# Kernel optimization log

Hardware: AMD Instinct MI355X
Metric: run time of the kernel (lower is better)

The kernel has to match this reference:

```python
import jax, jax.numpy as jnp
import numpy as np

HIDDEN = 1024
IN = 256
OUT = 256
DT_OVER_TAU = 0.05  # dt=0.05, tau=1


def setup_inputs() -> dict:
    key = jax.random.key(0)
    k0, k1, k2, k3 = jax.random.split(key, 4)
    g = 0.9
    x = jax.random.normal(k0, (512, 64, IN), dtype=jnp.float32)  # (tsq, batch, n_input)
    Win = jax.random.normal(k1, (IN, HIDDEN), dtype=jnp.float32) * (1.0 / HIDDEN)
    Wr = jax.random.normal(k2, (HIDDEN, HIDDEN), dtype=jnp.float32) * (g * g / HIDDEN)
    bias = jnp.zeros((1, HIDDEN), dtype=jnp.float32)
    Wout = jax.random.normal(k3, (HIDDEN, OUT), dtype=jnp.float32) * (1.0 / HIDDEN)
    return {"x": x, "Win": Win, "Wr": Wr, "bias": bias, "Wout": Wout}


def reference(x, Win, Wr, bias, Wout):
    tsq, batch, _ = x.shape
    a = DT_OVER_TAU
    # input projection: (batch, tsq, hidden)
    input_proj = jnp.einsum('tbi,ih->bth', x, Win)
    h0 = jnp.zeros((batch, HIDDEN), dtype=x.dtype)

    def step(h, ip_t):  # ip_t: (batch, hidden)
        h_new = (1.0 - a) * h + a * (jnp.tanh(h) @ Wr + ip_t + bias)
        return h_new, h_new

    # scan over time (time-major input_proj)
    _, hiddens_tm = jax.lax.scan(step, h0, jnp.swapaxes(input_proj, 0, 1))  # (tsq, batch, hidden)
    tot_rnnhid = jnp.swapaxes(hiddens_tm, 0, 1)           # (batch, tsq, hidden)
    rnn_out = jnp.tanh(tot_rnnhid)
    tot_output = rnn_out @ Wout                            # (batch, tsq, out)
    output_tensor = jnp.swapaxes(tot_output, 0, 1)         # (tsq, batch, out)
    return (output_tensor, input_proj, tot_rnnhid, tot_output)
```

## Files before the change

### kernel.cpp

```cpp
#include <hip/hip_runtime.h>
#include <cstdint>
#include <cstddef>


typedef short bf16x8 __attribute__((ext_vector_type(8)));
typedef float f32x4  __attribute__((ext_vector_type(4)));
typedef int   int4v  __attribute__((ext_vector_type(4)));

#define O1_OFF 8388608UL
#define O2_OFF 41943040UL
#define O3_OFF 75497472UL

#define SENT 0x7F80
#define SENT2 0x7F807F80

__device__ __forceinline__ unsigned short f2bf(float f) {
    unsigned u = __float_as_uint(f);
    u += 0x7FFFu + ((u >> 16) & 1u);
    return (unsigned short)(u >> 16);
}

__device__ __forceinline__ float fast_tanh(float x) {
    float e = __builtin_amdgcn_exp2f(2.8853900817779268f * x);
    return 1.0f - 2.0f * __builtin_amdgcn_rcpf(e + 1.0f);
}

__global__ void poison_y(int* __restrict__ o0, int* __restrict__ o3)
{
    const int flat = blockIdx.x * 256 + threadIdx.x;
    int4v p = {SENT2, SENT2, SENT2, SENT2};
#pragma unroll
    for (int c = 0; c < 4; ++c) {
        size_t off = (size_t)c * 2097152 + (size_t)flat * 4;
        __builtin_nontemporal_store(p, (int4v*)(o0 + off));
        __builtin_nontemporal_store(p, (int4v*)(o3 + off));
    }
}

__global__ void prep_transpose(const float* __restrict__ Win, const float* __restrict__ Wout,
                               unsigned short* __restrict__ winT, unsigned short* __restrict__ woutT)
{
    __shared__ float tbuf[64 * 65];
    const int tid = threadIdx.x;
    const int bx = blockIdx.x;
    const float* src; unsigned short* dst; int k0, n0, srcld, dstld;
    if (bx < 64) { int tk = bx & 3, tn = bx >> 2; k0 = tk * 64; n0 = tn * 64; src = Win;  srcld = 1024; dst = winT;  dstld = 256; }
    else         { int b2 = bx - 64; int tk = b2 >> 2, tn = b2 & 3; k0 = tk * 64; n0 = tn * 64; src = Wout; srcld = 256;  dst = woutT; dstld = 1024; }

    for (int it = 0; it < 16; ++it) {
        int flat = it * 256 + tid;
        int k = flat >> 6, nn = flat & 63;
        tbuf[k * 65 + nn] = src[(size_t)(k0 + k) * srcld + n0 + nn];
    }
    __syncthreads();
    int* d32 = (int*)dst;
    for (int it = 0; it < 8; ++it) {
        int flat = it * 256 + tid;
        int nn = flat >> 5, kd = flat & 31;
        float v0 = tbuf[(2 * kd) * 65 + nn];
        float v1 = tbuf[(2 * kd + 1) * 65 + nn];
        d32[(size_t)(n0 + nn) * (dstld / 2) + (k0 / 2) + kd] = (int)(f2bf(v0) | ((unsigned)f2bf(v1) << 16));
    }
}

__launch_bounds__(256, 1)
__global__ void input_proj_kernel(const float* __restrict__ x, const unsigned short* __restrict__ winT,
                                  float* __restrict__ ip)
{
    extern __shared__ short lds[];
    short* win_s = lds;
    short* x_s   = lds + 256 * 264;
    const int tid = threadIdx.x;
    const int lane = tid & 63, wv = tid >> 6;
    const int nslice = blockIdx.x & 3;
    const int wgm = blockIdx.x >> 2;
    const int n0 = nslice * 256;
    const int n = lane & 15, q = lane >> 4;

    {
        const int* src = (const int*)winT;
        int* dstl = (int*)win_s;
        for (int it = 0; it < 128; ++it) {
            int flat = it * 256 + tid;
            int nn = flat >> 7, kd = flat & 127;
            dstl[nn * 132 + kd] = src[(size_t)(n0 + nn) * 128 + kd];
        }
    }
    __syncthreads();

    const int msub = (wv & 1) * 16;
    const int ntbase = (wv >> 1) * 8;

    for (int i = 0; i < 16; ++i) {
        int mt = wgm * 16 + i;
        int r0 = mt * 32;
        {
            for (int it = 0; it < 16; ++it) {
                int flat = it * 256 + tid;
                int rr = flat >> 7, kp = flat & 127;
                const float* xp = x + (size_t)(r0 + rr) * 256 + kp * 2;
                ((int*)x_s)[rr * 132 + kp] = (int)(f2bf(xp[0]) | ((unsigned)f2bf(xp[1]) << 16));
            }
        }
        __syncthreads();

        f32x4 acc[8] = {};
#pragma unroll
        for (int kc = 0; kc < 8; ++kc) {
            bf16x8 af = *(const bf16x8*)(x_s + (msub + n) * 264 + kc * 32 + q * 8);
#pragma unroll
            for (int u = 0; u < 8; ++u) {
                bf16x8 bfv = *(const bf16x8*)(win_s + ((ntbase + u) * 16 + n) * 264 + kc * 32 + q * 8);
                acc[u] = __builtin_amdgcn_mfma_f32_16x16x32_bf16(af, bfv, acc[u], 0, 0, 0);
            }
        }
#pragma unroll
        for (int u = 0; u < 8; ++u) {
            int ncol = n0 + (ntbase + u) * 16 + n;
#pragma unroll
            for (int rr = 0; rr < 4; ++rr) {
                int R = r0 + msub + q * 4 + rr;
                int t = R >> 6, b = R & 63;
                ip[((size_t)b * 512 + t) * 1024 + ncol] = acc[u][rr];
            }
        }
        __syncthreads();
    }
}

__launch_bounds__(256, 1)
__global__ void rnn_scan(const float* __restrict__ Wr, const float* __restrict__ bias,
                         const float* __restrict__ ip, float* __restrict__ hout,
                         char* ybase0, char* ybase3)
{
    __shared__ short y_lds[4 * 1032];
    const int tid = threadIdx.x;
    const int lane = tid & 63;
    const int bx = blockIdx.x;
    const int j = bx >> 3;
    const int g = (bx & 7) + 8 * (j & 1);
    const int w = j >> 1;
    const int b0 = g * 4;
    const int colbase = w * 64 + (tid >> 6) * 16;
    const int n = lane & 15;
    const int q = lane >> 4;
    const int col = colbase + n;

    bf16x8 wrf[32];
#pragma unroll
    for (int kc = 0; kc < 32; ++kc) {
        int kbase = kc * 32 + q * 8;
        union { bf16x8 v; unsigned short u[8]; } tmp;
#pragma unroll
        for (int jj = 0; jj < 8; ++jj)
            tmp.u[jj] = f2bf(Wr[(size_t)(kbase + jj) * 1024 + col]);
        wrf[kc] = tmp.v;
    }
    const float biasv = bias[col];

    float h[4] = {0.f, 0.f, 0.f, 0.f};
    int gaveup = 0;
    const int r = tid >> 6;
    const int c0 = tid & 63;

    for (int t = 0; t < 512; ++t) {
        float ipv[4] = {0.f, 0.f, 0.f, 0.f};
        if (lane < 16) {
#pragma unroll
            for (int rr = 0; rr < 4; ++rr)
                ipv[rr] = __builtin_nontemporal_load(ip + ((size_t)(b0 + rr) * 512 + t) * 1024 + col);
        }

        f32x4 acc0 = {0.f, 0.f, 0.f, 0.f}, acc1 = {0.f, 0.f, 0.f, 0.f};
        if (t > 0) {
            const int* ysrc = (const int*)((t - 1) < 256 ? (ybase0 + (size_t)(t - 1) * 131072)
                                                         : (ybase3 + (size_t)(t - 1 - 256) * 131072));
            const int* bsrc = ysrc + (b0 + r) * 512 + c0;
            int* yl = (int*)y_lds + r * 516 + c0;
            int vals[8];
            if (!gaveup) {
                unsigned pend = 0xFFu;
                int spins = 0;
                while (true) {
#pragma unroll
                    for (int it = 0; it < 8; ++it)
                        if (pend & (1u << it))
                            vals[it] = __hip_atomic_load(bsrc + it * 64, __ATOMIC_RELAXED, __HIP_MEMORY_SCOPE_AGENT);
#pragma unroll
                    for (int it = 0; it < 8; ++it)
                        if (pend & (1u << it)) {
                            int v = vals[it];
                            if ((v & 0xFFFF) != SENT && ((v >> 16) & 0xFFFF) != SENT)
                                pend &= ~(1u << it);
                        }
                    if (pend == 0) break;
                    if (__builtin_expect(++spins > (1 << 16), 0)) { gaveup = 1; break; }
                    __builtin_amdgcn_s_sleep(1);
                }
            } else {
#pragma unroll
                for (int it = 0; it < 8; ++it)
                    vals[it] = __hip_atomic_load(bsrc + it * 64, __ATOMIC_RELAXED, __HIP_MEMORY_SCOPE_AGENT);
            }
#pragma unroll
            for (int it = 0; it < 8; ++it)
                yl[it * 64] = vals[it];
            __syncthreads();

#pragma unroll
            for (int kc = 0; kc < 32; kc += 2) {
                bf16x8 a0, a1;
                if (n < 4) {
                    a0 = *(const bf16x8*)(y_lds + n * 1032 + kc * 32 + q * 8);
                    a1 = *(const bf16x8*)(y_lds + n * 1032 + (kc + 1) * 32 + q * 8);
                } else { a0 = (bf16x8)0; a1 = (bf16x8)0; }
                acc0 = __builtin_amdgcn_mfma_f32_16x16x32_bf16(a0, wrf[kc],     acc0, 0, 0, 0);
                acc1 = __builtin_amdgcn_mfma_f32_16x16x32_bf16(a1, wrf[kc + 1], acc1, 0, 0, 0);
            }
        }

#pragma unroll
        for (int rr = 0; rr < 4; ++rr) {
            float rv = acc0[rr] + acc1[rr];
            h[rr] = 0.95f * h[rr] + 0.05f * (rv + ipv[rr] + biasv);
        }

        if (lane < 16) {
            char* ydst = (t < 256) ? (ybase0 + (size_t)t * 131072) : (ybase3 + (size_t)(t - 256) * 131072);
            unsigned short* yp = (unsigned short*)ydst;
#pragma unroll
            for (int rr = 0; rr < 4; ++rr) {
                unsigned short yb = f2bf(fast_tanh(h[rr]));
                __hip_atomic_store(yp + (b0 + rr) * 1024 + col, yb,
                                   __ATOMIC_RELAXED, __HIP_MEMORY_SCOPE_AGENT);
            }
#pragma unroll
            for (int rr = 0; rr < 4; ++rr)
                __builtin_nontemporal_store(h[rr], hout + ((size_t)(b0 + rr) * 512 + t) * 1024 + col);
        }
        __syncthreads();
    }
}

__launch_bounds__(256, 1)
__global__ void out_proj_kernel(const float* __restrict__ h, const unsigned short* __restrict__ woutT,
                                float* __restrict__ out0, float* __restrict__ out3)
{
    extern __shared__ short lds[];
    const int tid = threadIdx.x;
    const int lane = tid & 63, wv = tid >> 6;
    const int R0 = blockIdx.x * 64;
    const int n = lane & 15, q = lane >> 4;
    f32x4 acc[16] = {};

    for (int kb = 0; kb < 8; ++kb) {
        {
            const int* src = (const int*)woutT;
            int* dstl = (int*)lds;
#pragma unroll
            for (int it = 0; it < 64; ++it) {
                int flat = it * 256 + tid;
                int nn = flat >> 6, kd = flat & 63;
                dstl[nn * 68 + kd] = src[(size_t)nn * 512 + kb * 64 + kd];
            }
        }
        __syncthreads();

        const int row = R0 + wv * 16 + n;
#pragma unroll
        for (int kc = 0; kc < 4; ++kc) {
            int k = kb * 128 + kc * 32 + q * 8;
            const float* hp = h + (size_t)row * 1024 + k;
            union { bf16x8 v; unsigned short u[8]; } af;
#pragma unroll
            for (int jj = 0; jj < 8; ++jj) af.u[jj] = f2bf(fast_tanh(hp[jj]));
#pragma unroll
            for (int u2 = 0; u2 < 16; ++u2) {
                bf16x8 bfv = *(const bf16x8*)(lds + (u2 * 16 + n) * 136 + kc * 32 + q * 8);
                acc[u2] = __builtin_amdgcn_mfma_f32_16x16x32_bf16(af.v, bfv, acc[u2], 0, 0, 0);
            }
        }
        __syncthreads();
    }
#pragma unroll
    for (int u2 = 0; u2 < 16; ++u2) {
        int ncol = u2 * 16 + n;
#pragma unroll
        for (int rr = 0; rr < 4; ++rr) {
            int R = R0 + wv * 16 + q * 4 + rr;
            int b = R >> 9, t = R & 511;
            float v = acc[u2][rr];
            out3[(size_t)R * 256 + ncol] = v;
            out0[((size_t)t * 64 + b) * 256 + ncol] = v;
        }
    }
}

extern "C" void kernel_launch(void* const* d_in, const int* in_sizes, int n_in,
                              void* d_out, int out_size, void* d_ws, size_t ws_size,
                              hipStream_t stream)
{
    const float* x    = (const float*)d_in[0];
    const float* Win  = (const float*)d_in[1];
    const float* Wr   = (const float*)d_in[2];
    const float* bias = (const float*)d_in[3];
    const float* Wout = (const float*)d_in[4];
    float* out = (float*)d_out;
    float* o0 = out;
    float* o1 = out + O1_OFF;
    float* o2 = out + O2_OFF;
    float* o3 = out + O3_OFF;

    unsigned short* winT  = (unsigned short*)d_ws;
    unsigned short* woutT = (unsigned short*)((char*)d_ws + 524288);

    hipFuncSetAttribute((const void*)input_proj_kernel, hipFuncAttributeMaxDynamicSharedMemorySize, 152064);
    hipFuncSetAttribute((const void*)out_proj_kernel,   hipFuncAttributeMaxDynamicSharedMemorySize, 69632);

    hipLaunchKernelGGL(poison_y, dim3(2048), dim3(256), 0, stream, (int*)o0, (int*)o3);
    hipLaunchKernelGGL(prep_transpose, dim3(128), dim3(256), 0, stream, Win, Wout, winT, woutT);
    hipLaunchKernelGGL(input_proj_kernel, dim3(256), dim3(256), 152064, stream, x, winT, o1);

    hipLaunchKernelGGL(rnn_scan, dim3(256), dim3(256), 0, stream,
                       Wr, bias, o1, o2, (char*)o0, (char*)o3);

    hipLaunchKernelGGL(out_proj_kernel, dim3(512), dim3(256), 69632, stream, o2, woutT, o0, o3);
}
```

Measured before the change: 2.434 ms.

## Double-buffer LDS, vectorize polling loads, pack bf16 stores, prefetch next ip

The recurrent scan kernel now polls the previous step's hidden state with two 16-byte cache-bypassing loads per thread instead of eight 4-byte atomic loads. It sleeps only after a few failed spins. The LDS staging buffer is double-buffered, which lets the trailing per-step __syncthreads be removed. Each pair of neighbouring lanes packs its two bf16 values into one 32-bit store, halving the number of cross-block stores. The input projection for step t+1 is prefetched after the current step so its load latency leaves the critical path. The inline asm and the sentinel checks at 32-bit granularity depend on stores staying whole-word.

```diff
diff --git a/kernel.cpp b/kernel.cpp
--- a/kernel.cpp
+++ b/kernel.cpp
@@ -11,7 +11,7 @@
 #define O2_OFF 41943040UL
 #define O3_OFF 75497472UL
 
-#define SENT 0x7F80
+#define SENT  0x7F80
 #define SENT2 0x7F807F80
 
 __device__ __forceinline__ unsigned short f2bf(float f) {
@@ -133,7 +133,7 @@
                          const float* __restrict__ ip, float* __restrict__ hout,
                          char* ybase0, char* ybase3)
 {
-    __shared__ short y_lds[4 * 1032];
+    __shared__ int y_lds[2][4][516];
     const int tid = threadIdx.x;
     const int lane = tid & 63;
     const int bx = blockIdx.x;
@@ -160,59 +160,47 @@
 
     float h[4] = {0.f, 0.f, 0.f, 0.f};
     int gaveup = 0;
-    const int r = tid >> 6;
-    const int c0 = tid & 63;
+    const int r  = tid >> 6;
+    const int c8 = (tid & 63) * 8;
+
+    float ipv[4] = {0.f, 0.f, 0.f, 0.f};
+    if (lane < 16) {
+#pragma unroll
+        for (int rr = 0; rr < 4; ++rr)
+            ipv[rr] = __builtin_nontemporal_load(ip + ((size_t)(b0 + rr) * 512 + 0) * 1024 + col);
+    }
 
     for (int t = 0; t < 512; ++t) {
-        float ipv[4] = {0.f, 0.f, 0.f, 0.f};
-        if (lane < 16) {
-#pragma unroll
-            for (int rr = 0; rr < 4; ++rr)
-                ipv[rr] = __builtin_nontemporal_load(ip + ((size_t)(b0 + rr) * 512 + t) * 1024 + col);
-        }
-
         f32x4 acc0 = {0.f, 0.f, 0.f, 0.f}, acc1 = {0.f, 0.f, 0.f, 0.f};
         if (t > 0) {
             const int* ysrc = (const int*)((t - 1) < 256 ? (ybase0 + (size_t)(t - 1) * 131072)
                                                          : (ybase3 + (size_t)(t - 1 - 256) * 131072));
-            const int* bsrc = ysrc + (b0 + r) * 512 + c0;
-            int* yl = (int*)y_lds + r * 516 + c0;
-            int vals[8];
-            if (!gaveup) {
-                unsigned pend = 0xFFu;
-                int spins = 0;
-                while (true) {
-#pragma unroll
-                    for (int it = 0; it < 8; ++it)
-                        if (pend & (1u << it))
-                            vals[it] = __hip_atomic_load(bsrc + it * 64, __ATOMIC_RELAXED, __HIP_MEMORY_SCOPE_AGENT);
-#pragma unroll
-                    for (int it = 0; it < 8; ++it)
-                        if (pend & (1u << it)) {
-                            int v = vals[it];
-                            if ((v & 0xFFFF) != SENT && ((v >> 16) & 0xFFFF) != SENT)
-                                pend &= ~(1u << it);
-                        }
-                    if (pend == 0) break;
-                    if (__builtin_expect(++spins > (1 << 16), 0)) { gaveup = 1; break; }
-                    __builtin_amdgcn_s_sleep(1);
-                }
-            } else {
-#pragma unroll
-                for (int it = 0; it < 8; ++it)
-                    vals[it] = __hip_atomic_load(bsrc + it * 64, __ATOMIC_RELAXED, __HIP_MEMORY_SCOPE_AGENT);
-            }
-#pragma unroll
-            for (int it = 0; it < 8; ++it)
-                yl[it * 64] = vals[it];
+            const int* bsrc = ysrc + (b0 + r) * 512 + c8;
+            int4v va, vb;
+            int spins = 0;
+            while (true) {
+                asm volatile(
+                    "global_load_dwordx4 %0, %2, off sc0 sc1\n\t"
+                    "global_load_dwordx4 %1, %2, off offset:16 sc0 sc1\n\t"
+                    "s_waitcnt vmcnt(0)"
+                    : "=&v"(va), "=&v"(vb) : "v"(bsrc) : "memory");
+                bool ok = (va[0] != SENT2) && (va[1] != SENT2) && (va[2] != SENT2) && (va[3] != SENT2)
+                       && (vb[0] != SENT2) && (vb[1] != SENT2) && (vb[2] != SENT2) && (vb[3] != SENT2);
+                if (ok || gaveup) break;
+                if (__builtin_expect(++spins > (1 << 16), 0)) { gaveup = 1; break; }
+                if (spins > 8) __builtin_amdgcn_s_sleep(1);
+            }
+            *(int4v*)&y_lds[t & 1][r][c8]     = va;
+            *(int4v*)&y_lds[t & 1][r][c8 + 4] = vb;
             __syncthreads();
 
+            const short* ybuf = (const short*)y_lds[t & 1];
 #pragma unroll
             for (int kc = 0; kc < 32; kc += 2) {
                 bf16x8 a0, a1;
                 if (n < 4) {
-                    a0 = *(const bf16x8*)(y_lds + n * 1032 + kc * 32 + q * 8);
-                    a1 = *(const bf16x8*)(y_lds + n * 1032 + (kc + 1) * 32 + q * 8);
+                    a0 = *(const bf16x8*)(ybuf + n * 1032 + kc * 32 + q * 8);
+                    a1 = *(const bf16x8*)(ybuf + n * 1032 + (kc + 1) * 32 + q * 8);
                 } else { a0 = (bf16x8)0; a1 = (bf16x8)0; }
                 acc0 = __builtin_amdgcn_mfma_f32_16x16x32_bf16(a0, wrf[kc],     acc0, 0, 0, 0);
                 acc1 = __builtin_amdgcn_mfma_f32_16x16x32_bf16(a1, wrf[kc + 1], acc1, 0, 0, 0);
@@ -225,20 +213,33 @@
             h[rr] = 0.95f * h[rr] + 0.05f * (rv + ipv[rr] + biasv);
         }
 
+        {
+            char* ydst = (t < 256) ? (ybase0 + (size_t)t * 131072) : (ybase3 + (size_t)(t - 256) * 131072);
+            int* ypd = (int*)ydst;
+            int mybf[4];
+#pragma unroll
+            for (int rr = 0; rr < 4; ++rr)
+                mybf[rr] = (int)f2bf(fast_tanh(h[rr]));
+#pragma unroll
+            for (int rr = 0; rr < 4; ++rr) {
+                int pbf = __shfl_xor(mybf[rr], 1);
+                if (lane < 16 && (n & 1) == 0) {
+                    int dv = mybf[rr] | (pbf << 16);
+                    __hip_atomic_store(ypd + (b0 + rr) * 512 + (col >> 1), dv,
+                                       __ATOMIC_RELAXED, __HIP_MEMORY_SCOPE_AGENT);
+                }
+            }
+        }
         if (lane < 16) {
-            char* ydst = (t < 256) ? (ybase0 + (size_t)t * 131072) : (ybase3 + (size_t)(t - 256) * 131072);
-            unsigned short* yp = (unsigned short*)ydst;
-#pragma unroll
-            for (int rr = 0; rr < 4; ++rr) {
-                unsigned short yb = f2bf(fast_tanh(h[rr]));
-                __hip_atomic_store(yp + (b0 + rr) * 1024 + col, yb,
-                                   __ATOMIC_RELAXED, __HIP_MEMORY_SCOPE_AGENT);
-            }
 #pragma unroll
             for (int rr = 0; rr < 4; ++rr)
                 __builtin_nontemporal_store(h[rr], hout + ((size_t)(b0 + rr) * 512 + t) * 1024 + col);
         }
-        __syncthreads();
+        if (t < 511 && lane < 16) {
+#pragma unroll
+            for (int rr = 0; rr < 4; ++rr)
+                ipv[rr] = __builtin_nontemporal_load(ip + ((size_t)(b0 + rr) * 512 + (t + 1)) * 1024 + col);
+        }
     }
 }
 
```

New measurement: 2.455 ms. No clear change (+0.8%).
